# Kernel tuning notes

Measured on AMD Instinct MI355X. Metric: run time of the kernel, lower is better.

The kernel has to match this reference:

```python
import jax, jax.numpy as jnp
import numpy as np


def _silu(x):
    return x * jax.nn.sigmoid(x)


def _ln(x, w, b, eps=1e-5):
    mu = x.mean(-1, keepdims=True)
    xc = x - mu
    var = (xc * xc).mean(-1, keepdims=True)
    return xc * jax.lax.rsqrt(var + eps) * w + b


def _segsum(a):
    # a: (..., Q) -> (..., Q, Q) lower-triangular cumulative segment sums
    Q = a.shape[-1]
    cs = jnp.cumsum(a, axis=-1)
    ss = cs[..., :, None] - cs[..., None, :]
    mask = jnp.tril(jnp.ones((Q, Q), dtype=bool))
    return jnp.where(mask, ss, -jnp.inf)


def _ssd(x, A, Bm, Cm, chunk=64):
    # Mamba2 SSD dual (chunked) form. x:(b,l,h,p) pre-scaled by dt, A:(b,l,h)=dt*A, Bm/Cm:(b,l,n)
    b, l, h, p = x.shape
    c = l // chunk
    x = x.reshape(b, c, chunk, h, p)
    A = A.reshape(b, c, chunk, h).transpose(0, 3, 1, 2)          # (b,h,c,q)
    Bm = Bm.reshape(b, c, chunk, -1)
    Cm = Cm.reshape(b, c, chunk, -1)
    Acs = jnp.cumsum(A, axis=-1)                                  # (b,h,c,q)
    Lmat = jnp.exp(_segsum(A))                                    # (b,h,c,q,q)
    Yd = jnp.einsum('bcln,bcsn,bhcls,bcshp->bclhp', Cm, Bm, Lmat, x)
    dec = jnp.exp(Acs[..., -1:] - Acs)                            # (b,h,c,q)
    states = jnp.einsum('bcln,bhcl,bclhp->bchpn', Bm, dec, x)     # (b,c,h,p,n)
    cdec = jnp.exp(Acs[..., -1]).transpose(2, 0, 1)               # (c,b,h)
    st = states.transpose(1, 0, 2, 3, 4)                          # (c,b,h,p,n)

    def step(carry, inp):
        s, d = inp
        return carry * d[..., None, None] + s, carry

    _, prev = jax.lax.scan(step, jnp.zeros_like(st[0]), (st, cdec))
    prev = prev.transpose(1, 0, 2, 3, 4)                          # (b,c,h,p,n)
    Yo = jnp.einsum('bcln,bchpn,bhcl->bclhp', Cm, prev, jnp.exp(Acs))
    return (Yd + Yo).reshape(b, l, h, p)


def _mamba(x, in_w, in_b, conv_w, conv_b, A_log, D, dt_bias, rms_w, out_w, headdim, d_state):
    b, l, _ = x.shape
    nh = A_log.shape[0]
    di = nh * headdim
    zxbcdt = x @ in_w.T + in_b
    z = zxbcdt[..., :di]
    xBC = zxbcdt[..., di:2 * di + 2 * d_state]
    dt = jax.nn.softplus(zxbcdt[..., -nh:] + dt_bias)             # (b,l,nh)
    K = conv_w.shape[-1]
    xp = jnp.pad(xBC, ((0, 0), (K - 1, 0), (0, 0)))               # causal depthwise conv
    xBC = sum(xp[:, k:k + l, :] * conv_w[:, k] for k in range(K))
    xBC = _silu(xBC + conv_b)
    xs = xBC[..., :di].reshape(b, l, nh, headdim)
    Bm = xBC[..., di:di + d_state]
    Cm = xBC[..., di + d_state:]
    A = -jnp.exp(A_log)
    y = _ssd(xs * dt[..., None], dt * A, Bm, Cm)
    y = y + D[None, None, :, None] * xs
    y = y.reshape(b, l, di) * _silu(z)                            # gated RMSNorm
    y = y * jax.lax.rsqrt(jnp.mean(y * y, -1, keepdims=True) + 1e-5) * rms_w
    return y @ out_w.T


def setup_inputs() -> dict:
    key = jax.random.key(0)
    ks = iter(jax.random.split(key, 64))

    def nrm(shape, s):
        return jax.random.normal(next(ks), shape, jnp.float32) * s

    d = {}
    d['x'] = jax.random.normal(next(ks), (4, 128, 64, 64), jnp.float32)
    d['seed_tok_w'] = nrm((8, 128), 0.08)
    d['seed_tok_b'] = jnp.zeros((8,), jnp.float32)
    d['seed_detok_w'] = nrm((128, 8), 0.3)
    d['seed_detok_b'] = jnp.zeros((128,), jnp.float32)
    d['sm_in_w'] = nrm((66, 8), 0.3)
    d['sm_in_b'] = jnp.zeros((66,), jnp.float32)
    d['sm_conv_w'] = nrm((48, 3), 0.3)
    d['sm_conv_b'] = jnp.zeros((48,), jnp.float32)
    d['sm_A_log'] = jnp.log(jnp.arange(1, 3, dtype=jnp.float32))
    d['sm_D'] = jnp.ones((2,), jnp.float32)
    d['sm_dt_bias'] = jnp.full((2,), -4.0, jnp.float32)
    d['sm_rms_w'] = jnp.ones((16,), jnp.float32)
    d['sm_out_w'] = nrm((8, 16), 0.2)
    d['cm_in_w'] = nrm((2, 196, 16), 0.2)
    d['cm_in_b'] = jnp.zeros((2, 196), jnp.float32)
    d['cm_conv_w'] = nrm((2, 160, 3), 0.3)
    d['cm_conv_b'] = jnp.zeros((2, 160), jnp.float32)
    d['cm_A_log'] = jnp.tile(jnp.log(jnp.arange(1, 5, dtype=jnp.float32)), (2, 1))
    d['cm_D'] = jnp.ones((2, 4), jnp.float32)
    d['cm_dt_bias'] = jnp.full((2, 4), -4.0, jnp.float32)
    d['cm_rms_w'] = jnp.ones((2, 32), jnp.float32)
    d['cm_out_w'] = nrm((2, 16, 32), 0.15)
    d['cross_W'] = jnp.eye(8, dtype=jnp.float32) + 0.01 * jax.random.normal(next(ks), (8, 8), jnp.float32)
    d['norm1_w'] = jnp.ones((128,), jnp.float32)
    d['norm1_b'] = jnp.zeros((128,), jnp.float32)
    d['norm2_w'] = jnp.ones((128,), jnp.float32)
    d['norm2_b'] = jnp.zeros((128,), jnp.float32)
    d['fc1_w'] = nrm((256, 128), 0.08)
    d['fc1_b'] = jnp.zeros((256,), jnp.float32)
    d['dw_w'] = nrm((256, 1, 3, 3), 0.2)
    d['dw_b'] = jnp.zeros((256,), jnp.float32)
    d['fc2_w'] = nrm((128, 256), 0.06)
    d['fc2_b'] = jnp.zeros((128,), jnp.float32)
    d['skip_scale'] = jnp.ones((1,), jnp.float32)
    return d


def reference(x, seed_tok_w, seed_tok_b, seed_detok_w, seed_detok_b,
              sm_in_w, sm_in_b, sm_conv_w, sm_conv_b, sm_A_log, sm_D, sm_dt_bias, sm_rms_w, sm_out_w,
              cm_in_w, cm_in_b, cm_conv_w, cm_conv_b, cm_A_log, cm_D, cm_dt_bias, cm_rms_w, cm_out_w,
              cross_W, norm1_w, norm1_b, norm2_w, norm2_b,
              fc1_w, fc1_b, dw_w, dw_b, fc2_w, fc2_b, skip_scale):
    B, C, H, W = x.shape
    L = H * W
    # --- GlobalSeed ---
    g = jnp.einsum('bchw,gc->bghw', x, seed_tok_w) + seed_tok_b[None, :, None, None]
    gf = g.reshape(B, -1, L).transpose(0, 2, 1)                   # (B,L,G)
    gf = _mamba(gf, sm_in_w, sm_in_b, sm_conv_w, sm_conv_b, sm_A_log, sm_D,
                sm_dt_bias, sm_rms_w, sm_out_w, 8, 16) + gf
    det = jnp.einsum('blg,cg->blc', gf, seed_detok_w) + seed_detok_b
    seed = x + det.transpose(0, 2, 1).reshape(B, C, H, W)
    # --- split-channel cascaded SSD (shared weights across splits) ---
    xn = _ln(x.reshape(B, C, L).transpose(0, 2, 1), norm1_w, norm1_b)   # (B,L,C)
    S = cross_W.shape[0]
    xs = jnp.stack(jnp.split(xn, S, axis=-1))                     # (S,B,L,C/S)

    def cascade(xi):
        for i in range(cm_in_w.shape[0]):
            xi = _mamba(xi, cm_in_w[i], cm_in_b[i], cm_conv_w[i], cm_conv_b[i],
                        cm_A_log[i], cm_D[i], cm_dt_bias[i], cm_rms_w[i], cm_out_w[i], 8, 64)
        return xi

    ys = jax.vmap(cascade)(xs) + xs * skip_scale
    # --- SubCrossToken mixing ---
    gm = ys.mean(axis=2)                                          # (S,B,Cs)
    wsm = jax.nn.softmax(cross_W, axis=1)
    gmix = jnp.einsum('qbc,qp->pbc', gm, wsm)
    ys = ys + gmix[:, :, None, :]
    out = ys.transpose(1, 2, 0, 3).reshape(B, L, -1)
    out = _ln(out, norm2_w, norm2_b)
    out = out.transpose(0, 2, 1).reshape(B, C, H, W) + seed
    # --- ConvFFN ---
    h1 = jnp.einsum('bchw,oc->bohw', out, fc1_w) + fc1_b[None, :, None, None]
    dw = jax.lax.conv_general_dilated(h1, dw_w, (1, 1), 'SAME',
                                      feature_group_count=h1.shape[1],
                                      dimension_numbers=('NCHW', 'OIHW', 'NCHW'))
    h2 = jax.nn.gelu(dw + dw_b[None, :, None, None])
    ffn = jnp.einsum('bohw,co->bchw', h2, fc2_w) + fc2_b[None, :, None, None]
    return out + ffn
```

## Files before the change

kernel.cpp:

```cpp
#include <hip/hip_runtime.h>
#include <math.h>

#define B_ 4
#define CCH 128
#define HH 64
#define WW 64
#define LL 4096
#define NCHK 64

__device__ __forceinline__ float siluf(float x) { return x / (1.f + __expf(-x)); }
__device__ __forceinline__ float softplusf(float x) { return (x > 20.f) ? x : log1pf(__expf(x)); }
__device__ __forceinline__ int swz(int n, int l) {
  return (n << 6) + ((((l >> 2) ^ ((n >> 2) & 15)) << 2) | (l & 3));
}

__global__ __launch_bounds__(256) void k_seedtok(const float* __restrict__ x,
    const float* __restrict__ w, const float* __restrict__ bias, float* __restrict__ gf)
{
  __shared__ float sw[8*128];
  int tid = threadIdx.x;
  for (int i = tid; i < 1024; i += 256) sw[i] = w[i];
  __syncthreads();
  int idx = blockIdx.x * 256 + tid;
  int b = idx / LL, l = idx % LL;
  const float* xp = x + (size_t)b*CCH*LL + l;
  float acc[8];
#pragma unroll
  for (int g = 0; g < 8; ++g) acc[g] = bias[g];
  for (int c = 0; c < CCH; ++c) {
    float xv = xp[(size_t)c*LL];
#pragma unroll
    for (int g = 0; g < 8; ++g) acc[g] += xv * sw[g*128 + c];
  }
  float* o = gf + (size_t)idx*8;
#pragma unroll
  for (int g = 0; g < 8; ++g) o[g] = acc[g];
}

template<int DIN, int NZ, int NDS, int NDT>
__global__ __launch_bounds__(256) void k_inproj(
    const float* __restrict__ src, int srcMode,
    const float* __restrict__ in_w, const float* __restrict__ in_b,
    const float* __restrict__ conv_w, const float* __restrict__ conv_b,
    const float* __restrict__ dt_bias,
    float* __restrict__ zb, float* __restrict__ dtb,
    float* __restrict__ xsb, float* __restrict__ Bb, float* __restrict__ Cb)
{
  constexpr int NXBC = NZ + 2*NDS;
  constexpr int NTOT = 2*NZ + 2*NDS + NDT;
  constexpr int NZQ  = NZ/4;
  constexpr int NDSQ = NDS/4;
  constexpr int XP   = DIN + 1;
  __shared__ float xt[66*XP];
  __shared__ float wl[NTOT*DIN];
  __shared__ float cwl[NXBC*3];
  __shared__ float cbl[NXBC];
  __shared__ float ibl[NTOT];
  __shared__ float dts[64*NDT];
  __shared__ float hp[NXBC*2];
  int tid = threadIdx.x;
  int seq = blockIdx.x >> 6;
  int l0  = (blockIdx.x & 63) << 6;
  for (int i = tid; i < NTOT*DIN; i += 256) wl[i] = in_w[i];
  for (int i = tid; i < NXBC*3; i += 256) cwl[i] = conv_w[i];
  for (int i = tid; i < NXBC; i += 256) cbl[i] = conv_b[i];
  for (int i = tid; i < NTOT; i += 256) ibl[i] = in_b[i];
  const float* sp; int sstr;
  if (srcMode == 0) { sp = src + (size_t)seq*LL*DIN; sstr = DIN; }
  else { sp = src + (size_t)(seq & 3)*LL*CCH + (seq >> 2)*16; sstr = CCH; }
  for (int i = tid; i < 66*DIN; i += 256) {
    int r = i / DIN, d = i % DIN;
    int l = l0 - 2 + r;
    xt[r*XP + d] = (l >= 0) ? sp[(size_t)l*sstr + d] : 0.f;
  }
  __syncthreads();
  for (int i = tid; i < 2*NXBC; i += 256) {
    int t = i & 1, ch = i >> 1;
    const float* wr = &wl[(NZ + ch)*DIN];
    const float* xp = &xt[t*XP];
    float acc = 0.f;
#pragma unroll
    for (int d = 0; d < DIN; ++d) acc += xp[d]*wr[d];
    hp[ch*2 + t] = acc;
  }
  __syncthreads();
  int l = tid & 63, w4 = tid >> 6;
  float xr2[DIN];
#pragma unroll
  for (int d = 0; d < DIN; ++d) xr2[d] = xt[(l+2)*XP + d];
  size_t gl = (size_t)seq*LL + l0 + l;
  int tok = l0 + l;
  float v0ok = (tok >= 2) ? 1.f : 0.f;
  float v1ok = (tok >= 1) ? 1.f : 0.f;
  {
    float zv[NZQ];
#pragma unroll
    for (int j = 0; j < NZQ; ++j) {
      int row = w4*NZQ + j;
      const float* wr = &wl[row*DIN];
      float acc = ibl[row];
#pragma unroll
      for (int d = 0; d < DIN; ++d) acc += xr2[d]*wr[d];
      zv[j] = acc;
    }
#pragma unroll
    for (int g = 0; g < NZQ/4; ++g)
      *(float4*)&zb[gl*NZ + w4*NZQ + 4*g] = make_float4(zv[4*g], zv[4*g+1], zv[4*g+2], zv[4*g+3]);
  }
  if (w4 < NDT) {
    int row = NTOT - NDT + w4;
    const float* wr = &wl[row*DIN];
    float acc = ibl[row] + dt_bias[w4];
#pragma unroll
    for (int d = 0; d < DIN; ++d) acc += xr2[d]*wr[d];
    dts[l*NDT + w4] = softplusf(acc);
  }
  auto convch = [&](int ch) -> float {
    int row = NZ + ch;
    const float* wr = &wl[row*DIN];
    float pm = 0.f;
#pragma unroll
    for (int d = 0; d < DIN; ++d) pm += xr2[d]*wr[d];
    float m1 = __shfl_up(pm, 1, 64);
    float m2 = __shfl_up(pm, 2, 64);
    float h0 = hp[ch*2 + 0], h1 = hp[ch*2 + 1];
    if (l == 0) m1 = h1;
    m2 = (l == 0) ? h0 : ((l == 1) ? h1 : m2);
    float ib = ibl[row];
    float conv = cbl[ch] + (m2+ib)*v0ok*cwl[ch*3+0] + (m1+ib)*v1ok*cwl[ch*3+1] + (pm+ib)*cwl[ch*3+2];
    return siluf(conv);
  };
  {
    float xv[NZQ];
#pragma unroll
    for (int j = 0; j < NZQ; ++j) xv[j] = convch(w4*NZQ + j);
#pragma unroll
    for (int g = 0; g < NZQ/4; ++g)
      *(float4*)&xsb[gl*NZ + w4*NZQ + 4*g] = make_float4(xv[4*g], xv[4*g+1], xv[4*g+2], xv[4*g+3]);
  }
  {
    float bv[NDSQ];
#pragma unroll
    for (int j = 0; j < NDSQ; ++j) bv[j] = convch(NZ + w4*NDSQ + j);
#pragma unroll
    for (int g = 0; g < NDSQ/4; ++g)
      *(float4*)&Bb[gl*NDS + w4*NDSQ + 4*g] = make_float4(bv[4*g], bv[4*g+1], bv[4*g+2], bv[4*g+3]);
  }
  {
    float cv[NDSQ];
#pragma unroll
    for (int j = 0; j < NDSQ; ++j) cv[j] = convch(NZ + NDS + w4*NDSQ + j);
#pragma unroll
    for (int g = 0; g < NDSQ/4; ++g)
      *(float4*)&Cb[gl*NDS + w4*NDSQ + 4*g] = make_float4(cv[4*g], cv[4*g+1], cv[4*g+2], cv[4*g+3]);
  }
  __syncthreads();
  if (tid < 64) {
    if constexpr (NDT == 4) {
      *(float4*)&dtb[((size_t)seq*LL + l0 + tid)*4] =
          make_float4(dts[tid*4], dts[tid*4+1], dts[tid*4+2], dts[tid*4+3]);
    } else {
      *(float2*)&dtb[((size_t)seq*LL + l0 + tid)*NDT] = make_float2(dts[tid*NDT], dts[tid*NDT+1]);
    }
  }
}

template<int DS, int NH>
__global__ __launch_bounds__(256) void k_ssd1(
    const float* __restrict__ xs, const float* __restrict__ dtb,
    const float* __restrict__ Bb, const float* __restrict__ Cb,
    const float* __restrict__ A_log,
    float* __restrict__ ybuf, float* __restrict__ states,
    float* __restrict__ cdec, float* __restrict__ acsOut)
{
  constexpr int DI = NH*8;
  constexpr int NG = DS/4;
  __shared__ __align__(16) float BtBl[DS*64];
  __shared__ __align__(16) float CtGt[64*64];
  __shared__ __align__(16) float xde[NH*64*8];
  __shared__ __align__(16) float xde2[NH*64*8];
  int tid = threadIdx.x;
  int cid = blockIdx.x & 63;
  int seq = blockIdx.x >> 6;
  int l0  = cid << 6;
  for (int i = tid; i < 16*DS; i += 256) {
    int ng = i % NG, l = i / NG;
    size_t g = ((size_t)seq*LL + l0 + l)*DS + 4*ng;
    float4 bv = *(const float4*)&Bb[g];
    float4 cv = *(const float4*)&Cb[g];
    BtBl[swz(4*ng+0, l)] = bv.x; BtBl[swz(4*ng+1, l)] = bv.y;
    BtBl[swz(4*ng+2, l)] = bv.z; BtBl[swz(4*ng+3, l)] = bv.w;
    CtGt[swz(4*ng+0, l)] = cv.x; CtGt[swz(4*ng+1, l)] = cv.y;
    CtGt[swz(4*ng+2, l)] = cv.z; CtGt[swz(4*ng+3, l)] = cv.w;
  }
  __syncthreads();
  int lt = (tid >> 4) << 2, st = (tid & 15) << 2;
  float acc[4][4] = {};
#pragma unroll 4
  for (int n = 0; n < DS; ++n) {
    float4 cv = *(const float4*)&CtGt[swz(n, lt)];
    float4 bv = *(const float4*)&BtBl[swz(n, st)];
    float cc[4] = {cv.x, cv.y, cv.z, cv.w};
    float bb[4] = {bv.x, bv.y, bv.z, bv.w};
#pragma unroll
    for (int i2 = 0; i2 < 4; ++i2)
#pragma unroll
      for (int j2 = 0; j2 < 4; ++j2)
        acc[i2][j2] += cc[i2]*bb[j2];
  }
  __syncthreads();
#pragma unroll
  for (int j = 0; j < 4; ++j) {
    float4 gv = make_float4(acc[0][j], acc[1][j], acc[2][j], acc[3][j]);
    *(float4*)&CtGt[swz(st + j, lt)] = gv;
  }
  for (int i = tid; i < 16*DS; i += 256) {
    int ng = i % NG, l = i / NG;
    float4 bv = *(const float4*)&Bb[((size_t)seq*LL + l0 + l)*DS + 4*ng];
    *(float4*)&BtBl[l*DS + 4*ng] = bv;
  }
  __syncthreads();
  int w = tid >> 6, lane = tid & 63;
  if (w < NH) {
    int h = w;
    float dt_l = dtb[((size_t)seq*LL + l0 + lane)*NH + h];
    float Aval = -__expf(A_log[h]);
    float v = dt_l * Aval;
#pragma unroll
    for (int off = 1; off < 64; off <<= 1) {
      float t = __shfl_up(v, off, 64);
      if (lane >= off) v += t;
    }
    float acs_l = v;
    float m = __shfl(v, 31, 64);
    float acsLast = __shfl(v, 63, 64);
    float el = __expf(fminf(acs_l - m, 60.f));
    float fl = __expf(fminf(m - acs_l, 60.f));
    float dec = __expf(acsLast - acs_l);
    const float* xp = &xs[((size_t)seq*LL + l0 + lane)*DI + h*8];
    float4 x0 = *(const float4*)xp, x1 = *(const float4*)(xp + 4);
    float s1 = dt_l*fl, s2 = dt_l*dec;
    float* xe = &xde[(h*64 + lane)*8];
    float* xf = &xde2[(h*64 + lane)*8];
    *(float4*)xe     = make_float4(x0.x*s1, x0.y*s1, x0.z*s1, x0.w*s1);
    *(float4*)(xe+4) = make_float4(x1.x*s1, x1.y*s1, x1.z*s1, x1.w*s1);
    *(float4*)xf     = make_float4(x0.x*s2, x0.y*s2, x0.z*s2, x0.w*s2);
    *(float4*)(xf+4) = make_float4(x1.x*s2, x1.y*s2, x1.z*s2, x1.w*s2);
    int lg = lane >> 2, lm = lane & 3;
    float ya[8] = {0,0,0,0,0,0,0,0};
#pragma unroll 4
    for (int s = 0; s < 64; ++s) {
      float g = CtGt[(s << 6) + ((((lg ^ ((s >> 2) & 15))) << 2) | lm)];
      g = (s <= lane) ? g : 0.f;
      const float* xr = &xde[(h*64 + s)*8];
      float4 a0 = *(const float4*)xr, a1 = *(const float4*)(xr + 4);
      ya[0] += g*a0.x; ya[1] += g*a0.y; ya[2] += g*a0.z; ya[3] += g*a0.w;
      ya[4] += g*a1.x; ya[5] += g*a1.y; ya[6] += g*a1.z; ya[7] += g*a1.w;
    }
    float* yp = &ybuf[((size_t)seq*LL + l0 + lane)*DI + h*8];
    *(float4*)yp     = make_float4(ya[0]*el, ya[1]*el, ya[2]*el, ya[3]*el);
    *(float4*)(yp+4) = make_float4(ya[4]*el, ya[5]*el, ya[6]*el, ya[7]*el);
    if (lane < DS) {
      float sa[8] = {0,0,0,0,0,0,0,0};
#pragma unroll 4
      for (int ll = 0; ll < 64; ++ll) {
        float b = BtBl[ll*DS + lane];
        const float* xr = &xde2[(h*64 + ll)*8];
        float4 a0 = *(const float4*)xr, a1 = *(const float4*)(xr + 4);
        sa[0] += b*a0.x; sa[1] += b*a0.y; sa[2] += b*a0.z; sa[3] += b*a0.w;
        sa[4] += b*a1.x; sa[5] += b*a1.y; sa[6] += b*a1.z; sa[7] += b*a1.w;
      }
      float* sp = &states[(((size_t)seq*NH + h)*NCHK + cid)*(size_t)(8*DS) + lane*8];
      *(float4*)sp     = make_float4(sa[0], sa[1], sa[2], sa[3]);
      *(float4*)(sp+4) = make_float4(sa[4], sa[5], sa[6], sa[7]);
    }
    if (lane == 63) cdec[((size_t)seq*NH + h)*NCHK + cid] = __expf(acsLast);
    acsOut[((size_t)seq*NH + h)*LL + l0 + lane] = acs_l;
  }
}

__global__ __launch_bounds__(512) void k_scan(float* __restrict__ st, const float* __restrict__ cd, int PN)
{
  int tid = threadIdx.x;
  size_t base = (size_t)blockIdx.x * NCHK * PN + tid;
  const float* c = cd + (size_t)blockIdx.x * NCHK;
  float carry = 0.f;
  for (int k = 0; k < NCHK; ++k) {
    size_t a = base + (size_t)k*PN;
    float s = st[a];
    st[a] = carry;
    carry = carry*c[k] + s;
  }
}

template<int DS, int NH>
__global__ __launch_bounds__(256) void k_ssd_yo(
    float* __restrict__ ybuf, const float* __restrict__ Cb,
    const float* __restrict__ prevSt, const float* __restrict__ acsG,
    const float* __restrict__ Dp, const float* __restrict__ xs)
{
  constexpr int DI = NH*8;
  constexpr int NG = DS/4;
  __shared__ __align__(16) float Ct2[DS*64];
  __shared__ __align__(16) float pvs[NH*DS*8];
  int tid = threadIdx.x;
  int cid = blockIdx.x & 63;
  int seq = blockIdx.x >> 6;
  int l0  = cid << 6;
  for (int i = tid; i < 16*DS; i += 256) {
    int ng = i % NG, l = i / NG;
    float4 cv = *(const float4*)&Cb[((size_t)seq*LL + l0 + l)*DS + 4*ng];
    Ct2[swz(4*ng+0, l)] = cv.x; Ct2[swz(4*ng+1, l)] = cv.y;
    Ct2[swz(4*ng+2, l)] = cv.z; Ct2[swz(4*ng+3, l)] = cv.w;
  }
  for (int i = tid; i < NH*DS*8; i += 256) {
    int h = i / (DS*8), r = i % (DS*8);
    pvs[i] = prevSt[(((size_t)seq*NH + h)*NCHK + cid)*(size_t)(DS*8) + r];
  }
  __syncthreads();
  int w = tid >> 6, lane = tid & 63;
  if (w < NH) {
    int h = w;
    float el = __expf(acsG[((size_t)seq*NH + h)*LL + l0 + lane]);
    float Dh = Dp[h];
    int lg = lane >> 2, lm = lane & 3;
    float acc[8] = {0,0,0,0,0,0,0,0};
#pragma unroll 4
    for (int n = 0; n < DS; ++n) {
      float c = Ct2[(n << 6) + ((((lg ^ ((n >> 2) & 15))) << 2) | lm)];
      const float* pr = &pvs[(h*DS + n)*8];
      float4 p0 = *(const float4*)pr, p1 = *(const float4*)(pr + 4);
      acc[0] += c*p0.x; acc[1] += c*p0.y; acc[2] += c*p0.z; acc[3] += c*p0.w;
      acc[4] += c*p1.x; acc[5] += c*p1.y; acc[6] += c*p1.z; acc[7] += c*p1.w;
    }
    size_t gi = ((size_t)seq*LL + l0 + lane)*DI + h*8;
    float4 y0 = *(const float4*)&ybuf[gi], y1 = *(const float4*)&ybuf[gi+4];
    float4 xv0 = *(const float4*)&xs[gi], xv1 = *(const float4*)&xs[gi+4];
    y0.x += el*acc[0] + Dh*xv0.x; y0.y += el*acc[1] + Dh*xv0.y;
    y0.z += el*acc[2] + Dh*xv0.z; y0.w += el*acc[3] + Dh*xv0.w;
    y1.x += el*acc[4] + Dh*xv1.x; y1.y += el*acc[5] + Dh*xv1.y;
    y1.z += el*acc[6] + Dh*xv1.z; y1.w += el*acc[7] + Dh*xv1.w;
    *(float4*)&ybuf[gi] = y0; *(float4*)&ybuf[gi+4] = y1;
  }
}

template<int DI, int DOUT>
__global__ __launch_bounds__(256) void k_gate(
    const float* __restrict__ ybuf, const float* __restrict__ zbuf,
    const float* __restrict__ rms_w, const float* __restrict__ out_w,
    float* __restrict__ dst, int resMode, const float* __restrict__ res,
    const float* __restrict__ skipPtr)
{
  __shared__ float ow[DOUT*DI];
  __shared__ float rw[DI];
  int tid = threadIdx.x;
  for (int i = tid; i < DOUT*DI; i += 256) ow[i] = out_w[i];
  for (int i = tid; i < DI; i += 256) rw[i] = rms_w[i];
  __syncthreads();
  size_t idx = (size_t)blockIdx.x*256 + tid;
  float y[DI];
  const float* yp = ybuf + idx*DI;
  const float* zp = zbuf + idx*DI;
  float ss = 0.f;
#pragma unroll
  for (int i = 0; i < DI; ++i) {
    float z = zp[i];
    float g = yp[i] * (z / (1.f + __expf(-z)));
    y[i] = g; ss += g*g;
  }
  float r = rsqrtf(ss*(1.f/DI) + 1e-5f);
#pragma unroll
  for (int i = 0; i < DI; ++i) y[i] *= r*rw[i];
  const float* rp = nullptr; float skip = 1.f;
  int seq = (int)(idx / LL), l = (int)(idx % LL);
  if (resMode == 1) rp = res + idx*DOUT;
  else if (resMode == 2) {
    int s = seq / B_, b = seq % B_;
    rp = res + ((size_t)b*LL + l)*CCH + s*DOUT;
    skip = skipPtr[0];
  }
  float* dp = dst + idx*DOUT;
#pragma unroll
  for (int o = 0; o < DOUT; ++o) {
    float acc = 0.f;
#pragma unroll
    for (int i = 0; i < DI; ++i) acc += y[i]*ow[o*DI + i];
    if (rp) acc += skip * rp[o];
    dp[o] = acc;
  }
}

__global__ __launch_bounds__(256) void k_detseed(const float* __restrict__ x,
    const float* __restrict__ gf2, const float* __restrict__ dw,
    const float* __restrict__ db, float* __restrict__ seed)
{
  size_t idx = (size_t)blockIdx.x*256 + threadIdx.x;
  int l = (int)(idx % LL); size_t t = idx / LL; int c = (int)(t % CCH); int b = (int)(t / CCH);
  const float* g = gf2 + ((size_t)b*LL + l)*8;
  float acc = db[c];
#pragma unroll
  for (int i = 0; i < 8; ++i) acc += g[i]*dw[c*8 + i];
  seed[idx] = x[idx] + acc;
}

__global__ __launch_bounds__(256) void k_ln1(const float* __restrict__ x,
    const float* __restrict__ w, const float* __restrict__ bb, float* __restrict__ xn)
{
  __shared__ float tile[128*65];
  __shared__ float mu[64], rs[64];
  int tid = threadIdx.x;
  int b = blockIdx.x >> 6;
  int l0 = (blockIdx.x & 63) << 6;
  for (int i = tid; i < 8192; i += 256) {
    int l = i & 63, c = i >> 6;
    tile[c*65 + l] = x[((size_t)b*CCH + c)*LL + l0 + l];
  }
  __syncthreads();
  if (tid < 64) {
    float s = 0.f;
    for (int c = 0; c < CCH; ++c) s += tile[c*65 + tid];
    float m = s * (1.f/CCH);
    float v = 0.f;
    for (int c = 0; c < CCH; ++c) { float d = tile[c*65 + tid] - m; v += d*d; }
    mu[tid] = m; rs[tid] = rsqrtf(v*(1.f/CCH) + 1e-5f);
  }
  __syncthreads();
  for (int i = tid; i < 8192; i += 256) {
    int c = i & 127, l = i >> 7;
    xn[((size_t)b*LL + l0 + l)*CCH + c] = (tile[c*65 + l] - mu[l])*rs[l]*w[c] + bb[c];
  }
}

__global__ __launch_bounds__(256) void k_gm(const float* __restrict__ ys, float* __restrict__ gm)
{
  __shared__ float red[256];
  int tid = threadIdx.x;
  int seq = blockIdx.x;
  int c = tid & 15, lane = tid >> 4;
  float s = 0.f;
  for (int l = lane; l < LL; l += 16) s += ys[((size_t)seq*LL + l)*16 + c];
  red[tid] = s;
  __syncthreads();
  if (tid < 16) {
    float t = 0.f;
    for (int g = 0; g < 16; ++g) t += red[g*16 + tid];
    gm[(size_t)seq*16 + tid] = t * (1.f/LL);
  }
}

__global__ __launch_bounds__(256) void k_mix(const float* __restrict__ gm,
    const float* __restrict__ crossW, float* __restrict__ gmix)
{
  __shared__ float wsm[64];
  int tid = threadIdx.x;
  if (tid < 8) {
    float mx = -1e30f;
    for (int p = 0; p < 8; ++p) mx = fmaxf(mx, crossW[tid*8 + p]);
    float e[8]; float s = 0.f;
    for (int p = 0; p < 8; ++p) { e[p] = __expf(crossW[tid*8 + p] - mx); s += e[p]; }
    for (int p = 0; p < 8; ++p) wsm[tid*8 + p] = e[p] / s;
  }
  __syncthreads();
  for (int i = tid; i < 512; i += 256) {
    int c = i & 15; int bb = (i >> 4) & 3; int p = i >> 6;
    float acc = 0.f;
    for (int q = 0; q < 8; ++q) acc += gm[((size_t)(q*B_ + bb))*16 + c] * wsm[q*8 + p];
    gmix[((size_t)(p*B_ + bb))*16 + c] = acc;
  }
}

__global__ __launch_bounds__(256) void k_out2(const float* __restrict__ ys,
    const float* __restrict__ gmix, const float* __restrict__ w, const float* __restrict__ bb,
    const float* __restrict__ seed, float* __restrict__ outb)
{
  __shared__ float tile[128*65];
  __shared__ float mu[64], rs[64];
  int tid = threadIdx.x;
  int b = blockIdx.x >> 6;
  int l0 = (blockIdx.x & 63) << 6;
  for (int i = tid; i < 8192; i += 256) {
    int c = i & 15; int l = (i >> 4) & 63; int s = i >> 10;
    int seq = s*B_ + b;
    tile[(s*16 + c)*65 + l] = ys[((size_t)seq*LL + l0 + l)*16 + c] + gmix[(size_t)seq*16 + c];
  }
  __syncthreads();
  if (tid < 64) {
    float sm = 0.f;
    for (int c = 0; c < 128; ++c) sm += tile[c*65 + tid];
    float m = sm * (1.f/128.f);
    float v = 0.f;
    for (int c = 0; c < 128; ++c) { float d = tile[c*65 + tid] - m; v += d*d; }
    mu[tid] = m; rs[tid] = rsqrtf(v*(1.f/128.f) + 1e-5f);
  }
  __syncthreads();
  for (int i = tid; i < 8192; i += 256) {
    int l = i & 63, c = i >> 6;
    size_t gi = ((size_t)b*CCH + c)*LL + l0 + l;
    outb[gi] = (tile[c*65 + l] - mu[l])*rs[l]*w[c] + bb[c] + seed[gi];
  }
}

__global__ __launch_bounds__(256) void k_fc1(const float* __restrict__ src,
    const float* __restrict__ w, const float* __restrict__ bias, float* __restrict__ dst)
{
  constexpr int WP = 129;
  __shared__ float st[128*64];
  __shared__ float wt[64*WP];
  int tid = threadIdx.x;
  int blk = blockIdx.x;
  int ot = blk & 3;
  int lt = (blk >> 2) & 63;
  int b  = blk >> 8;
  int l0 = lt << 6, o0 = ot << 6;
  for (int i = tid; i < 8192; i += 256) {
    int l = i & 63, c = i >> 6;
    st[c*64 + l] = src[((size_t)b*CCH + c)*LL + l0 + l];
  }
  for (int i = tid; i < 8192; i += 256) {
    int c = i & 127, o = i >> 7;
    wt[o*WP + c] = w[(size_t)(o0 + o)*128 + c];
  }
  __syncthreads();
  int l4 = (tid & 15) << 2, o4 = (tid >> 4) << 2;
  float a0[4] = {}, a1[4] = {}, a2[4] = {}, a3[4] = {};
#pragma unroll 4
  for (int c = 0; c < 128; ++c) {
    float4 sv = *(float4*)&st[c*64 + l4];
    float w0 = wt[(o4+0)*WP + c];
    float w1 = wt[(o4+1)*WP + c];
    float w2 = wt[(o4+2)*WP + c];
    float w3 = wt[(o4+3)*WP + c];
    a0[0] += w0*sv.x; a0[1] += w0*sv.y; a0[2] += w0*sv.z; a0[3] += w0*sv.w;
    a1[0] += w1*sv.x; a1[1] += w1*sv.y; a1[2] += w1*sv.z; a1[3] += w1*sv.w;
    a2[0] += w2*sv.x; a2[1] += w2*sv.y; a2[2] += w2*sv.z; a2[3] += w2*sv.w;
    a3[0] += w3*sv.x; a3[1] += w3*sv.y; a3[2] += w3*sv.z; a3[3] += w3*sv.w;
  }
  float* rows[4] = {a0, a1, a2, a3};
#pragma unroll
  for (int j = 0; j < 4; ++j) {
    int o = o0 + o4 + j;
    float bi = bias[o];
    float* a = rows[j];
    *(float4*)&dst[((size_t)b*256 + o)*LL + l0 + l4] =
        make_float4(a[0]+bi, a[1]+bi, a[2]+bi, a[3]+bi);
  }
}

__global__ __launch_bounds__(256) void k_dw(const float* __restrict__ h1,
    const float* __restrict__ w, const float* __restrict__ bias, float* __restrict__ h2)
{
  size_t idx = (size_t)blockIdx.x*256 + threadIdx.x;
  int col = (int)(idx % WW); size_t t = idx / WW; int row = (int)(t % HH);
  t /= HH; int ch = (int)(t % 256); int b = (int)(t / 256);
  const float* base = h1 + ((size_t)b*256 + ch)*LL;
  const float* wp = w + ch*9;
  float acc = 0.f;
#pragma unroll
  for (int di = 0; di < 3; ++di) {
    int i = row + di - 1; if (i < 0 || i >= HH) continue;
#pragma unroll
    for (int dj = 0; dj < 3; ++dj) {
      int j = col + dj - 1; if (j < 0 || j >= WW) continue;
      acc += base[i*WW + j]*wp[di*3 + dj];
    }
  }
  float v = acc + bias[ch];
  float u = 0.7978845608028654f*(v + 0.044715f*v*v*v);
  float e = __expf(2.f*u);
  float th = 1.f - 2.f/(e + 1.f);
  h2[idx] = 0.5f*v*(1.f + th);
}

__global__ __launch_bounds__(256) void k_fc2(const float* __restrict__ h2,
    const float* __restrict__ w, const float* __restrict__ bias,
    const float* __restrict__ resid, float* __restrict__ dst)
{
  constexpr int WP = 260;
  __shared__ float st[128*64];
  __shared__ float wt[32*WP];
  int tid = threadIdx.x;
  int blk = blockIdx.x;
  int ct = blk & 3;
  int lt = (blk >> 2) & 63;
  int b  = blk >> 8;
  int l0 = lt << 6, c0 = ct << 5;
  for (int i = tid; i < 32*256; i += 256) {
    int o = i & 255, c = i >> 8;
    wt[c*WP + o] = w[(size_t)(c0 + c)*256 + o];
  }
  int l4 = (tid & 15) << 2, c2 = (tid >> 4) << 1;
  float a0[4] = {}, a1[4] = {};
  for (int ko = 0; ko < 256; ko += 128) {
    __syncthreads();
    for (int i = tid; i < 8192; i += 256) {
      int l = i & 63, o = i >> 6;
      st[o*64 + l] = h2[((size_t)b*256 + ko + o)*LL + l0 + l];
    }
    __syncthreads();
#pragma unroll 4
    for (int o = 0; o < 128; ++o) {
      float4 sv = *(float4*)&st[o*64 + l4];
      float w0 = wt[(c2+0)*WP + ko + o];
      float w1 = wt[(c2+1)*WP + ko + o];
      a0[0] += w0*sv.x; a0[1] += w0*sv.y; a0[2] += w0*sv.z; a0[3] += w0*sv.w;
      a1[0] += w1*sv.x; a1[1] += w1*sv.y; a1[2] += w1*sv.z; a1[3] += w1*sv.w;
    }
  }
  float* rows[2] = {a0, a1};
#pragma unroll
  for (int j = 0; j < 2; ++j) {
    int c = c0 + c2 + j;
    float bi = bias[c];
    size_t gi = ((size_t)b*CCH + c)*LL + l0 + l4;
    float4 rv = *(const float4*)&resid[gi];
    float* a = rows[j];
    *(float4*)&dst[gi] = make_float4(a[0]+bi+rv.x, a[1]+bi+rv.y, a[2]+bi+rv.z, a[3]+bi+rv.w);
  }
}

extern "C" void kernel_launch(void* const* d_in, const int* in_sizes, int n_in,
                              void* d_out, int out_size, void* d_ws, size_t ws_size,
                              hipStream_t stream) {
  (void)in_sizes; (void)n_in; (void)out_size; (void)ws_size;
  const float* x        = (const float*)d_in[0];
  const float* tok_w    = (const float*)d_in[1];
  const float* tok_b    = (const float*)d_in[2];
  const float* detok_w  = (const float*)d_in[3];
  const float* detok_b  = (const float*)d_in[4];
  const float* sm_in_w  = (const float*)d_in[5];
  const float* sm_in_b  = (const float*)d_in[6];
  const float* sm_conv_w= (const float*)d_in[7];
  const float* sm_conv_b= (const float*)d_in[8];
  const float* sm_A_log = (const float*)d_in[9];
  const float* sm_D     = (const float*)d_in[10];
  const float* sm_dt_b  = (const float*)d_in[11];
  const float* sm_rms_w = (const float*)d_in[12];
  const float* sm_out_w = (const float*)d_in[13];
  const float* cm_in_w  = (const float*)d_in[14];
  const float* cm_in_b  = (const float*)d_in[15];
  const float* cm_conv_w= (const float*)d_in[16];
  const float* cm_conv_b= (const float*)d_in[17];
  const float* cm_A_log = (const float*)d_in[18];
  const float* cm_D     = (const float*)d_in[19];
  const float* cm_dt_b  = (const float*)d_in[20];
  const float* cm_rms_w = (const float*)d_in[21];
  const float* cm_out_w = (const float*)d_in[22];
  const float* cross_W  = (const float*)d_in[23];
  const float* n1w      = (const float*)d_in[24];
  const float* n1b      = (const float*)d_in[25];
  const float* n2w      = (const float*)d_in[26];
  const float* n2b      = (const float*)d_in[27];
  const float* fc1w     = (const float*)d_in[28];
  const float* fc1b     = (const float*)d_in[29];
  const float* dww      = (const float*)d_in[30];
  const float* dwb      = (const float*)d_in[31];
  const float* fc2w     = (const float*)d_in[32];
  const float* fc2b     = (const float*)d_in[33];
  const float* skp      = (const float*)d_in[34];
  float* ws  = (float*)d_ws;
  float* out = (float*)d_out;

  const size_t SEED = 0;
  const size_t XN   = 2097152;
  const size_t YS   = 4194304;
  const size_t OUTB = 6291456;
  const size_t GM   = 8388608;
  const size_t GMIX = 8389120;
  const size_t SCR  = 8389632;
  const size_t CZ   = SCR;
  const size_t CDT  = CZ   + 4194304;
  const size_t CXS  = CDT  + 524288;
  const size_t CBF  = CXS  + 4194304;
  const size_t CCF  = CBF  + 8388608;
  const size_t CACS = CCF  + 8388608;
  const size_t CST  = CACS + 2097152;
  const size_t CCD  = CST  + 4194304;
  const size_t CY   = CCD  + 8192;
  const size_t XB   = CY   + 4194304;
  const size_t SGF  = SCR;
  const size_t SZ   = SCR + 131072;
  const size_t SDT  = SCR + 393216;
  const size_t SXS  = SCR + 425984;
  const size_t SB   = SCR + 688128;
  const size_t SC   = SCR + 950272;
  const size_t SACS = SCR + 1212416;
  const size_t SST  = SCR + 1245184;
  const size_t SCD  = SCR + 1310720;
  const size_t SY   = SCR + 1311232;
  const size_t SOUT = SCR + 1573376;
  const size_t H1 = SCR;
  const size_t H2 = SCR + 4194304;

  k_seedtok<<<64, 256, 0, stream>>>(x, tok_w, tok_b, ws + SGF);
  k_inproj<8,16,16,2><<<B_*64, 256, 0, stream>>>(ws + SGF, 0, sm_in_w, sm_in_b, sm_conv_w,
      sm_conv_b, sm_dt_b, ws + SZ, ws + SDT, ws + SXS, ws + SB, ws + SC);
  k_ssd1<16,2><<<B_*NCHK, 256, 0, stream>>>(ws + SXS, ws + SDT, ws + SB, ws + SC,
      sm_A_log, ws + SY, ws + SST, ws + SCD, ws + SACS);
  k_scan<<<B_*2, 128, 0, stream>>>(ws + SST, ws + SCD, 128);
  k_ssd_yo<16,2><<<B_*NCHK, 256, 0, stream>>>(ws + SY, ws + SC, ws + SST, ws + SACS, sm_D, ws + SXS);
  k_gate<16,8><<<B_*LL/256, 256, 0, stream>>>(ws + SY, ws + SZ, sm_rms_w, sm_out_w,
      ws + SOUT, 1, ws + SGF, skp);
  k_detseed<<<B_*CCH*LL/256, 256, 0, stream>>>(x, ws + SOUT, detok_w, detok_b, ws + SEED);

  k_ln1<<<B_*64, 256, 0, stream>>>(x, n1w, n1b, ws + XN);

  k_inproj<16,32,64,4><<<32*64, 256, 0, stream>>>(ws + XN, 1, cm_in_w, cm_in_b, cm_conv_w,
      cm_conv_b, cm_dt_b, ws + CZ, ws + CDT, ws + CXS, ws + CBF, ws + CCF);
  k_ssd1<64,4><<<32*NCHK, 256, 0, stream>>>(ws + CXS, ws + CDT, ws + CBF, ws + CCF,
      cm_A_log, ws + CY, ws + CST, ws + CCD, ws + CACS);
  k_scan<<<32*4, 512, 0, stream>>>(ws + CST, ws + CCD, 512);
  k_ssd_yo<64,4><<<32*NCHK, 256, 0, stream>>>(ws + CY, ws + CCF, ws + CST, ws + CACS, cm_D, ws + CXS);
  k_gate<32,16><<<32*LL/256, 256, 0, stream>>>(ws + CY, ws + CZ, cm_rms_w, cm_out_w,
      ws + XB, 0, nullptr, skp);

  k_inproj<16,32,64,4><<<32*64, 256, 0, stream>>>(ws + XB, 0, cm_in_w + 3136, cm_in_b + 196,
      cm_conv_w + 480, cm_conv_b + 160, cm_dt_b + 4, ws + CZ, ws + CDT, ws + CXS, ws + CBF, ws + CCF);
  k_ssd1<64,4><<<32*NCHK, 256, 0, stream>>>(ws + CXS, ws + CDT, ws + CBF, ws + CCF,
      cm_A_log + 4, ws + CY, ws + CST, ws + CCD, ws + CACS);
  k_scan<<<32*4, 512, 0, stream>>>(ws + CST, ws + CCD, 512);
  k_ssd_yo<64,4><<<32*NCHK, 256, 0, stream>>>(ws + CY, ws + CCF, ws + CST, ws + CACS, cm_D + 4, ws + CXS);
  k_gate<32,16><<<32*LL/256, 256, 0, stream>>>(ws + CY, ws + CZ, cm_rms_w + 32, cm_out_w + 512,
      ws + YS, 2, ws + XN, skp);

  k_gm<<<32, 256, 0, stream>>>(ws + YS, ws + GM);
  k_mix<<<1, 256, 0, stream>>>(ws + GM, cross_W, ws + GMIX);
  k_out2<<<B_*64, 256, 0, stream>>>(ws + YS, ws + GMIX, n2w, n2b, ws + SEED, ws + OUTB);

  k_fc1<<<B_*64*4, 256, 0, stream>>>(ws + OUTB, fc1w, fc1b, ws + H1);
  k_dw<<<B_*256*LL/256, 256, 0, stream>>>(ws + H1, dww, dwb, ws + H2);
  k_fc2<<<B_*64*4, 256, 0, stream>>>(ws + H2, fc2w, fc2b, ws + OUTB, out);
}
```

Baseline: 654.7 us.

## Fuse detokenize into out2, tile depthwise conv in LDS, share SSD scaled-x buffer

The separate detokenize+seed kernel is removed. Its 8-wide projection plus the residual x are now computed inside k_out2, which avoids writing and rereading a full-size seed tensor. The depthwise 3x3 conv now loads a padded 66x66 plane into shared memory, one block per channel plane, and each thread computes 16 outputs, cutting redundant global loads. In k_ssd1 the second scaled-x buffer is dropped: states reuse the fl-scaled x and are rescaled by exp(acsLast-m), which saves LDS and stores but can lose precision, because fl is clamped at exp(60).

```diff
diff --git a/kernel.cpp b/kernel.cpp
--- a/kernel.cpp
+++ b/kernel.cpp
@@ -178,7 +178,6 @@
   __shared__ __align__(16) float BtBl[DS*64];
   __shared__ __align__(16) float CtGt[64*64];
   __shared__ __align__(16) float xde[NH*64*8];
-  __shared__ __align__(16) float xde2[NH*64*8];
   int tid = threadIdx.x;
   int cid = blockIdx.x & 63;
   int seq = blockIdx.x >> 6;
@@ -236,16 +235,12 @@
     float acsLast = __shfl(v, 63, 64);
     float el = __expf(fminf(acs_l - m, 60.f));
     float fl = __expf(fminf(m - acs_l, 60.f));
-    float dec = __expf(acsLast - acs_l);
     const float* xp = &xs[((size_t)seq*LL + l0 + lane)*DI + h*8];
     float4 x0 = *(const float4*)xp, x1 = *(const float4*)(xp + 4);
-    float s1 = dt_l*fl, s2 = dt_l*dec;
+    float s1 = dt_l*fl;
     float* xe = &xde[(h*64 + lane)*8];
-    float* xf = &xde2[(h*64 + lane)*8];
     *(float4*)xe     = make_float4(x0.x*s1, x0.y*s1, x0.z*s1, x0.w*s1);
     *(float4*)(xe+4) = make_float4(x1.x*s1, x1.y*s1, x1.z*s1, x1.w*s1);
-    *(float4*)xf     = make_float4(x0.x*s2, x0.y*s2, x0.z*s2, x0.w*s2);
-    *(float4*)(xf+4) = make_float4(x1.x*s2, x1.y*s2, x1.z*s2, x1.w*s2);
     int lg = lane >> 2, lm = lane & 3;
     float ya[8] = {0,0,0,0,0,0,0,0};
 #pragma unroll 4
@@ -261,18 +256,19 @@
     *(float4*)yp     = make_float4(ya[0]*el, ya[1]*el, ya[2]*el, ya[3]*el);
     *(float4*)(yp+4) = make_float4(ya[4]*el, ya[5]*el, ya[6]*el, ya[7]*el);
     if (lane < DS) {
+      float r2 = __expf(acsLast - m);
       float sa[8] = {0,0,0,0,0,0,0,0};
 #pragma unroll 4
       for (int ll = 0; ll < 64; ++ll) {
         float b = BtBl[ll*DS + lane];
-        const float* xr = &xde2[(h*64 + ll)*8];
+        const float* xr = &xde[(h*64 + ll)*8];
         float4 a0 = *(const float4*)xr, a1 = *(const float4*)(xr + 4);
         sa[0] += b*a0.x; sa[1] += b*a0.y; sa[2] += b*a0.z; sa[3] += b*a0.w;
         sa[4] += b*a1.x; sa[5] += b*a1.y; sa[6] += b*a1.z; sa[7] += b*a1.w;
       }
-      float* sp = &states[(((size_t)seq*NH + h)*NCHK + cid)*(size_t)(8*DS) + lane*8];
-      *(float4*)sp     = make_float4(sa[0], sa[1], sa[2], sa[3]);
-      *(float4*)(sp+4) = make_float4(sa[4], sa[5], sa[6], sa[7]);
+      float* sp2 = &states[(((size_t)seq*NH + h)*NCHK + cid)*(size_t)(8*DS) + lane*8];
+      *(float4*)sp2     = make_float4(sa[0]*r2, sa[1]*r2, sa[2]*r2, sa[3]*r2);
+      *(float4*)(sp2+4) = make_float4(sa[4]*r2, sa[5]*r2, sa[6]*r2, sa[7]*r2);
     }
     if (lane == 63) cdec[((size_t)seq*NH + h)*NCHK + cid] = __expf(acsLast);
     acsOut[((size_t)seq*NH + h)*LL + l0 + lane] = acs_l;
@@ -390,19 +386,6 @@
   }
 }
 
-__global__ __launch_bounds__(256) void k_detseed(const float* __restrict__ x,
-    const float* __restrict__ gf2, const float* __restrict__ dw,
-    const float* __restrict__ db, float* __restrict__ seed)
-{
-  size_t idx = (size_t)blockIdx.x*256 + threadIdx.x;
-  int l = (int)(idx % LL); size_t t = idx / LL; int c = (int)(t % CCH); int b = (int)(t / CCH);
-  const float* g = gf2 + ((size_t)b*LL + l)*8;
-  float acc = db[c];
-#pragma unroll
-  for (int i = 0; i < 8; ++i) acc += g[i]*dw[c*8 + i];
-  seed[idx] = x[idx] + acc;
-}
-
 __global__ __launch_bounds__(256) void k_ln1(const float* __restrict__ x,
     const float* __restrict__ w, const float* __restrict__ bb, float* __restrict__ xn)
 {
@@ -471,7 +454,9 @@
 
 __global__ __launch_bounds__(256) void k_out2(const float* __restrict__ ys,
     const float* __restrict__ gmix, const float* __restrict__ w, const float* __restrict__ bb,
-    const float* __restrict__ seed, float* __restrict__ outb)
+    const float* __restrict__ x, const float* __restrict__ gf2,
+    const float* __restrict__ dw, const float* __restrict__ db,
+    float* __restrict__ outb)
 {
   __shared__ float tile[128*65];
   __shared__ float mu[64], rs[64];
@@ -493,10 +478,20 @@
     mu[tid] = m; rs[tid] = rsqrtf(v*(1.f/128.f) + 1e-5f);
   }
   __syncthreads();
+  int lfix = tid & 63;
+  float g8[8];
+  {
+    const float* gp = gf2 + ((size_t)b*LL + l0 + lfix)*8;
+#pragma unroll
+    for (int k = 0; k < 8; ++k) g8[k] = gp[k];
+  }
   for (int i = tid; i < 8192; i += 256) {
     int l = i & 63, c = i >> 6;
     size_t gi = ((size_t)b*CCH + c)*LL + l0 + l;
-    outb[gi] = (tile[c*65 + l] - mu[l])*rs[l]*w[c] + bb[c] + seed[gi];
+    float det = db[c];
+#pragma unroll
+    for (int k = 0; k < 8; ++k) det += g8[k]*dw[c*8 + k];
+    outb[gi] = (tile[c*65 + l] - mu[l])*rs[l]*w[c] + bb[c] + x[gi] + det;
   }
 }
 
@@ -549,26 +544,36 @@
 __global__ __launch_bounds__(256) void k_dw(const float* __restrict__ h1,
     const float* __restrict__ w, const float* __restrict__ bias, float* __restrict__ h2)
 {
-  size_t idx = (size_t)blockIdx.x*256 + threadIdx.x;
-  int col = (int)(idx % WW); size_t t = idx / WW; int row = (int)(t % HH);
-  t /= HH; int ch = (int)(t % 256); int b = (int)(t / 256);
-  const float* base = h1 + ((size_t)b*256 + ch)*LL;
-  const float* wp = w + ch*9;
-  float acc = 0.f;
-#pragma unroll
-  for (int di = 0; di < 3; ++di) {
-    int i = row + di - 1; if (i < 0 || i >= HH) continue;
-#pragma unroll
-    for (int dj = 0; dj < 3; ++dj) {
-      int j = col + dj - 1; if (j < 0 || j >= WW) continue;
-      acc += base[i*WW + j]*wp[di*3 + dj];
-    }
-  }
-  float v = acc + bias[ch];
-  float u = 0.7978845608028654f*(v + 0.044715f*v*v*v);
-  float e = __expf(2.f*u);
-  float th = 1.f - 2.f/(e + 1.f);
-  h2[idx] = 0.5f*v*(1.f + th);
+  __shared__ float tile[66*66];
+  int tid = threadIdx.x;
+  int blk = blockIdx.x;
+  const float* base = h1 + (size_t)blk*LL;
+  const float* wp = w + (blk & 255)*9;
+  float bi = bias[blk & 255];
+  for (int i = tid; i < 66*66; i += 256) {
+    int r = i / 66, cc = i % 66;
+    int gr = r - 1, gc = cc - 1;
+    tile[i] = (gr >= 0 && gr < HH && gc >= 0 && gc < WW) ? base[gr*WW + gc] : 0.f;
+  }
+  float w00 = wp[0], w01 = wp[1], w02 = wp[2];
+  float w10 = wp[3], w11 = wp[4], w12 = wp[5];
+  float w20 = wp[6], w21 = wp[7], w22 = wp[8];
+  __syncthreads();
+  float* outp = h2 + (size_t)blk*LL;
+#pragma unroll
+  for (int k = 0; k < 16; ++k) {
+    int j = tid + k*256;
+    int row = j >> 6, col = j & 63;
+    const float* t0 = &tile[row*66 + col];
+    float acc = t0[0]*w00  + t0[1]*w01  + t0[2]*w02
+              + t0[66]*w10 + t0[67]*w11 + t0[68]*w12
+              + t0[132]*w20 + t0[133]*w21 + t0[134]*w22;
+    float v = acc + bi;
+    float u = 0.7978845608028654f*(v + 0.044715f*v*v*v);
+    float e = __expf(2.f*u);
+    float th = 1.f - 2.f/(e + 1.f);
+    outp[j] = 0.5f*v*(1.f + th);
+  }
 }
 
 __global__ __launch_bounds__(256) void k_fc2(const float* __restrict__ h2,
@@ -660,7 +665,8 @@
   float* ws  = (float*)d_ws;
   float* out = (float*)d_out;
 
-  const size_t SEED = 0;
+  const size_t SGF0 = 0;
+  const size_t SOUTn= 131072;
   const size_t XN   = 2097152;
   const size_t YS   = 4194304;
   const size_t OUTB = 6291456;
@@ -677,30 +683,27 @@
   const size_t CCD  = CST  + 4194304;
   const size_t CY   = CCD  + 8192;
   const size_t XB   = CY   + 4194304;
-  const size_t SGF  = SCR;
-  const size_t SZ   = SCR + 131072;
-  const size_t SDT  = SCR + 393216;
-  const size_t SXS  = SCR + 425984;
-  const size_t SB   = SCR + 688128;
-  const size_t SC   = SCR + 950272;
-  const size_t SACS = SCR + 1212416;
-  const size_t SST  = SCR + 1245184;
-  const size_t SCD  = SCR + 1310720;
-  const size_t SY   = SCR + 1311232;
-  const size_t SOUT = SCR + 1573376;
+  const size_t SZ   = SCR;
+  const size_t SDT  = SZ  + 262144;
+  const size_t SXS  = SDT + 32768;
+  const size_t SB   = SXS + 262144;
+  const size_t SC   = SB  + 262144;
+  const size_t SACS = SC  + 262144;
+  const size_t SST  = SACS + 32768;
+  const size_t SCD  = SST + 65536;
+  const size_t SY   = SCD + 512;
   const size_t H1 = SCR;
   const size_t H2 = SCR + 4194304;
 
-  k_seedtok<<<64, 256, 0, stream>>>(x, tok_w, tok_b, ws + SGF);
-  k_inproj<8,16,16,2><<<B_*64, 256, 0, stream>>>(ws + SGF, 0, sm_in_w, sm_in_b, sm_conv_w,
+  k_seedtok<<<64, 256, 0, stream>>>(x, tok_w, tok_b, ws + SGF0);
+  k_inproj<8,16,16,2><<<B_*64, 256, 0, stream>>>(ws + SGF0, 0, sm_in_w, sm_in_b, sm_conv_w,
       sm_conv_b, sm_dt_b, ws + SZ, ws + SDT, ws + SXS, ws + SB, ws + SC);
   k_ssd1<16,2><<<B_*NCHK, 256, 0, stream>>>(ws + SXS, ws + SDT, ws + SB, ws + SC,
       sm_A_log, ws + SY, ws + SST, ws + SCD, ws + SACS);
   k_scan<<<B_*2, 128, 0, stream>>>(ws + SST, ws + SCD, 128);
   k_ssd_yo<16,2><<<B_*NCHK, 256, 0, stream>>>(ws + SY, ws + SC, ws + SST, ws + SACS, sm_D, ws + SXS);
   k_gate<16,8><<<B_*LL/256, 256, 0, stream>>>(ws + SY, ws + SZ, sm_rms_w, sm_out_w,
-      ws + SOUT, 1, ws + SGF, skp);
-  k_detseed<<<B_*CCH*LL/256, 256, 0, stream>>>(x, ws + SOUT, detok_w, detok_b, ws + SEED);
+      ws + SOUTn, 1, ws + SGF0, skp);
 
   k_ln1<<<B_*64, 256, 0, stream>>>(x, n1w, n1b, ws + XN);
 
@@ -724,9 +727,10 @@
 
   k_gm<<<32, 256, 0, stream>>>(ws + YS, ws + GM);
   k_mix<<<1, 256, 0, stream>>>(ws + GM, cross_W, ws + GMIX);
-  k_out2<<<B_*64, 256, 0, stream>>>(ws + YS, ws + GMIX, n2w, n2b, ws + SEED, ws + OUTB);
+  k_out2<<<B_*64, 256, 0, stream>>>(ws + YS, ws + GMIX, n2w, n2b,
+      x, ws + SOUTn, detok_w, detok_b, ws + OUTB);
 
   k_fc1<<<B_*64*4, 256, 0, stream>>>(ws + OUTB, fc1w, fc1b, ws + H1);
-  k_dw<<<B_*256*LL/256, 256, 0, stream>>>(ws + H1, dww, dwb, ws + H2);
+  k_dw<<<B_*256, 256, 0, stream>>>(ws + H1, dww, dwb, ws + H2);
   k_fc2<<<B_*64*4, 256, 0, stream>>>(ws + H2, fc2w, fc2b, ws + OUTB, out);
 }
```

Result: no change. 647.1 us (-1.1%).
